# Kernel optimization log

Hardware: AMD Instinct MI355X
Metric: run time of the kernel (lower is better)

Reference implementation:

```python
import jax, jax.numpy as jnp
import numpy as np
import math

HIDDEN = 1024
ADAPTER = 256

def gelu_new(x):
    # BERT/GPT tanh-approx gelu, matches the torch code exactly
    return 0.5 * x * (1.0 + jnp.tanh(math.sqrt(2.0 / math.pi) * (x + 0.044715 * x ** 3)))

def setup_inputs() -> dict:
    key = jax.random.key(0)
    k1, k2, k3 = jax.random.split(key, 3)
    hidden_states = jax.random.normal(k1, (8, 4096, HIDDEN), dtype=jnp.float32)
    # LayerNorm params: weight=1, bias=0 per init_bert_weights
    ln_weight = jnp.ones((HIDDEN,), jnp.float32)
    ln_bias = jnp.zeros((HIDDEN,), jnp.float32)
    # Linear weights ~ N(0, 0.02), biases zero
    w_down = jax.random.normal(k2, (HIDDEN, ADAPTER), jnp.float32) * 0.02
    b_down = jnp.zeros((ADAPTER,), jnp.float32)
    w_up = jax.random.normal(k3, (ADAPTER, HIDDEN), jnp.float32) * 0.02
    b_up = jnp.zeros((HIDDEN,), jnp.float32)
    return {"hidden_states": hidden_states, "ln_weight": ln_weight, "ln_bias": ln_bias,
            "w_down": w_down, "b_down": b_down, "w_up": w_up, "b_up": b_up}

def layer_norm(x, weight, bias, eps=1e-5):
    mean = jnp.mean(x, axis=-1, keepdims=True)
    var = jnp.mean(jnp.square(x - mean), axis=-1, keepdims=True)
    return (x - mean) * jax.lax.rsqrt(var + eps) * weight + bias

def reference(hidden_states, ln_weight, ln_bias, w_down, b_down, w_up, b_up):
    h = layer_norm(hidden_states, ln_weight, ln_bias)           # [B,S,H]
    h = gelu_new(jnp.einsum('bsh,ha->bsa', h, w_down) + b_down)  # [B,S,A]
    h = jnp.einsum('bsa,ah->bsh', h, w_up) + b_up                # [B,S,H]
    return h + hidden_states
```

## Files before the change

kernel.cpp:

```cpp
#include <hip/hip_runtime.h>

#define HID 1024
#define ADP 256
#define MB  32

typedef short s16x8 __attribute__((ext_vector_type(8)));
typedef unsigned short u16x8 __attribute__((ext_vector_type(8)));
typedef float f32x4 __attribute__((ext_vector_type(4)));

__device__ __forceinline__ unsigned short f2bf(float f) {
    union { float f; unsigned int u; } v; v.f = f;
    unsigned int r = v.u + 0x7fffu + ((v.u >> 16) & 1u);
    return (unsigned short)(r >> 16);
}

__device__ __forceinline__ float bf2f(unsigned short u) {
    union { unsigned int u; float f; } v; v.u = ((unsigned int)u) << 16;
    return v.f;
}

__device__ __forceinline__ float gelu_new_f(float x) {
    float t = 0.7978845608028654f * x * (1.0f + 0.044715f * x * x);
    t = fminf(fmaxf(t, -15.f), 15.f);
    float e = __expf(-2.0f * t);
    float th = (1.0f - e) / (1.0f + e);
    return 0.5f * x * (1.0f + th);
}

__global__ void pack_b(const float* __restrict__ in, unsigned short* __restrict__ out,
                       const float* __restrict__ scale, int K, int N) {
    __shared__ unsigned short sh[32][72];
    int k0 = blockIdx.x * 32, n0 = blockIdx.y * 64;
    int t = threadIdx.x;
    int r = t >> 3, cg = t & 7;
    const float* src = in + (size_t)(k0 + r) * N + n0 + cg * 8;
    float sc = scale ? scale[k0 + r] : 1.0f;
    f32x4 v0 = *(const f32x4*)(src);
    f32x4 v1 = *(const f32x4*)(src + 4);
    #pragma unroll
    for (int e = 0; e < 4; ++e) {
        sh[r][cg * 8 + e]     = f2bf(sc * v0[e]);
        sh[r][cg * 8 + 4 + e] = f2bf(sc * v1[e]);
    }
    __syncthreads();
    int tile = t >> 6, l = t & 63, q = l >> 4, l15 = l & 15;
    u16x8 o;
    #pragma unroll
    for (int e = 0; e < 8; ++e)
        o[e] = sh[q * 8 + e][tile * 16 + l15];
    size_t tid_g = (size_t)(blockIdx.y * 4 + tile) * (K / 32) + blockIdx.x;
    *(u16x8*)(out + tid_g * 512 + (size_t)l * 8) = o;
}

__global__ void make_corr(const float* __restrict__ wd, const float* __restrict__ lnw,
                          const float* __restrict__ lnb, const float* __restrict__ bdn,
                          float* __restrict__ svec, float* __restrict__ tvec) {
    int w = threadIdx.x >> 6, lane = threadIdx.x & 63;
    int a = blockIdx.x * 4 + w;
    float sv = 0.f, tv = 0.f;
    #pragma unroll 4
    for (int i = 0; i < 16; ++i) {
        int h = lane + 64 * i;
        float wv_ = wd[(size_t)h * ADP + a];
        sv += bf2f(f2bf(lnw[h] * wv_));
        tv += lnb[h] * wv_;
    }
    #pragma unroll
    for (int s = 1; s < 64; s <<= 1) { sv += __shfl_xor(sv, s); tv += __shfl_xor(tv, s); }
    if (lane == 0) { svec[a] = sv; tvec[a] = bdn[a] + tv; }
}

__global__ __launch_bounds__(256, 4)
void adapter_fused(const float* __restrict__ x,
                   const float* __restrict__ bup,
                   const float* __restrict__ svec, const float* __restrict__ tvec,
                   const unsigned short* __restrict__ WdP,
                   const unsigned short* __restrict__ WuP,
                   float* __restrict__ out)
{
    __shared__ unsigned short a_h[MB][264];
    __shared__ float ep[4][16][68];
    __shared__ float stats[MB][2];
    __shared__ float sv_s[ADP], tv_s[ADP];

    const int tid  = threadIdx.x;
    const int wv   = tid >> 6;
    const int lane = tid & 63;
    const int q    = lane >> 4;
    const int l15  = lane & 15;
    const long row0 = (long)blockIdx.x * MB;

    sv_s[tid] = svec[tid];
    tv_s[tid] = tvec[tid];

    const int r   = tid >> 3;
    const int sub = tid & 7;

    f32x4 c1[2][4];
    #pragma unroll
    for (int a = 0; a < 2; ++a)
        #pragma unroll
        for (int b = 0; b < 4; ++b)
            c1[a][b] = (f32x4){0.f, 0.f, 0.f, 0.f};

    float sum1 = 0.f, sum2 = 0.f;

    f32x4 xv[8];
    {
        const f32x4* xr = (const f32x4*)(x + (row0 + r) * HID);
        #pragma unroll
        for (int i = 0; i < 8; ++i)
            xv[i] = __builtin_nontemporal_load(&xr[sub + 8 * i]);
    }

    for (int kc = 0; kc < 4; ++kc) {
        #pragma unroll
        for (int i = 0; i < 8; ++i) {
            int f4 = sub + 8 * i;
            f32x4 v = xv[i];
            sum1 += v[0] + v[1] + v[2] + v[3];
            sum2 += v[0] * v[0] + v[1] * v[1] + v[2] * v[2] + v[3] * v[3];
            ushort4 o;
            o.x = f2bf(v[0]); o.y = f2bf(v[1]); o.z = f2bf(v[2]); o.w = f2bf(v[3]);
            *(ushort4*)&a_h[r][f4 * 4] = o;
        }
        __syncthreads();
        if (kc < 3) {
            const f32x4* xr = (const f32x4*)(x + (row0 + r) * HID + (kc + 1) * 256);
            #pragma unroll
            for (int i = 0; i < 8; ++i)
                xv[i] = __builtin_nontemporal_load(&xr[sub + 8 * i]);
        }
        #pragma unroll
        for (int ks = 0; ks < 8; ++ks) {
            int kof = ks * 32 + q * 8;
            s16x8 af[2], bfr[4];
            af[0] = *(const s16x8*)&a_h[l15][kof];
            af[1] = *(const s16x8*)&a_h[16 + l15][kof];
            #pragma unroll
            for (int nt = 0; nt < 4; ++nt)
                bfr[nt] = *(const s16x8*)&WdP[(((size_t)(wv * 4 + nt) * 32) + kc * 8 + ks) * 512 + lane * 8];
            #pragma unroll
            for (int mt = 0; mt < 2; ++mt)
                #pragma unroll
                for (int nt = 0; nt < 4; ++nt)
                    c1[mt][nt] = __builtin_amdgcn_mfma_f32_16x16x32_bf16(af[mt], bfr[nt], c1[mt][nt], 0, 0, 0);
        }
        __syncthreads();
    }

    sum1 += __shfl_xor(sum1, 1); sum2 += __shfl_xor(sum2, 1);
    sum1 += __shfl_xor(sum1, 2); sum2 += __shfl_xor(sum2, 2);
    sum1 += __shfl_xor(sum1, 4); sum2 += __shfl_xor(sum2, 4);
    if (sub == 0) {
        float mean = sum1 * (1.f / HID);
        float var  = sum2 * (1.f / HID) - mean * mean;
        stats[r][0] = mean;
        stats[r][1] = rsqrtf(var + 1e-5f);
    }
    __syncthreads();

    #pragma unroll
    for (int mt = 0; mt < 2; ++mt)
        #pragma unroll
        for (int nt = 0; nt < 4; ++nt) {
            int a = wv * 64 + nt * 16 + l15;
            float sv = sv_s[a], tv = tv_s[a];
            #pragma unroll
            for (int rr = 0; rr < 4; ++rr) {
                int m = mt * 16 + q * 4 + rr;
                float mean = stats[m][0], rstd = stats[m][1];
                float c = rstd * (c1[mt][nt][rr] - mean * sv) + tv;
                a_h[m][a] = f2bf(gelu_new_f(c));
            }
        }
    __syncthreads();

    for (int ncc = 0; ncc < 4; ++ncc) {
        const int cb = wv * 256 + ncc * 64;
        f32x4 c2[2][4];
        #pragma unroll
        for (int a = 0; a < 2; ++a)
            #pragma unroll
            for (int b = 0; b < 4; ++b)
                c2[a][b] = (f32x4){0.f, 0.f, 0.f, 0.f};
        #pragma unroll
        for (int ks = 0; ks < 8; ++ks) {
            int kof = ks * 32 + q * 8;
            s16x8 af[2], bfr[4];
            af[0] = *(const s16x8*)&a_h[l15][kof];
            af[1] = *(const s16x8*)&a_h[16 + l15][kof];
            #pragma unroll
            for (int nt = 0; nt < 4; ++nt)
                bfr[nt] = *(const s16x8*)&WuP[(((size_t)(wv * 16 + ncc * 4 + nt) * 8) + ks) * 512 + lane * 8];
            #pragma unroll
            for (int mt = 0; mt < 2; ++mt)
                #pragma unroll
                for (int nt = 0; nt < 4; ++nt)
                    c2[mt][nt] = __builtin_amdgcn_mfma_f32_16x16x32_bf16(af[mt], bfr[nt], c2[mt][nt], 0, 0, 0);
        }
        #pragma unroll
        for (int mt = 0; mt < 2; ++mt) {
            #pragma unroll
            for (int nt = 0; nt < 4; ++nt)
                #pragma unroll
                for (int rr = 0; rr < 4; ++rr)
                    ep[wv][q * 4 + rr][nt * 16 + l15] = c2[mt][nt][rr];
            __builtin_amdgcn_s_waitcnt(0xc07f);
            int rr2 = lane >> 2, c4 = lane & 3;
            long gm = row0 + mt * 16 + rr2;
            const f32x4* xr = (const f32x4*)(x + gm * HID + cb);
            const f32x4* bu = (const f32x4*)(bup + cb);
            f32x4* orow     = (f32x4*)(out + gm * HID + cb);
            #pragma unroll
            for (int i = 0; i < 4; ++i) {
                int f4 = i * 4 + c4;
                f32x4 v  = *(const f32x4*)&ep[wv][rr2][f4 * 4];
                f32x4 rs = __builtin_nontemporal_load(&xr[f4]);
                f32x4 b4 = bu[f4];
                v += rs + b4;
                __builtin_nontemporal_store(v, &orow[f4]);
            }
            __builtin_amdgcn_s_waitcnt(0xc07f);
        }
    }
}

extern "C" void kernel_launch(void* const* d_in, const int* in_sizes, int n_in,
                              void* d_out, int out_size, void* d_ws, size_t ws_size,
                              hipStream_t stream) {
    const float* x   = (const float*)d_in[0];
    const float* lnw = (const float*)d_in[1];
    const float* lnb = (const float*)d_in[2];
    const float* wd  = (const float*)d_in[3];
    const float* bd  = (const float*)d_in[4];
    const float* wu  = (const float*)d_in[5];
    const float* bu  = (const float*)d_in[6];
    float* out = (float*)d_out;

    unsigned short* WdP = (unsigned short*)d_ws;
    unsigned short* WuP = WdP + (size_t)HID * ADP;
    float* svec = (float*)(WuP + (size_t)HID * ADP);
    float* tvec = svec + ADP;

    pack_b<<<dim3(HID / 32, ADP / 64), 256, 0, stream>>>(wd, WdP, lnw, HID, ADP);
    pack_b<<<dim3(ADP / 32, HID / 64), 256, 0, stream>>>(wu, WuP, nullptr, ADP, HID);
    make_corr<<<ADP / 4, 256, 0, stream>>>(wd, lnw, lnb, bd, svec, tvec);

    const int rows = in_sizes[0] / HID;
    adapter_fused<<<rows / MB, 256, 0, stream>>>(x, bu, svec, tvec, WdP, WuP, out);
}
```

Baseline: 338.9 us.

## Merge prep kernels and double fused-kernel block to 512 threads with direct epilogue

The three weight-preparation launches are merged into a single prep kernel, and the correction-vector pass now runs as one serial block. The fused adapter kernel moves from 256 to 512 threads per block, so each wave owns half as many output columns in both GEMMs and the per-wave accumulator registers shrink. The LDS staging epilogue is dropped in favour of scalar residual loads and stores straight from the MFMA layout. Input loads lose their nontemporal hint. The aim is more waves in flight and fewer launches, at the cost of narrower, less coalesced epilogue accesses and a slow serial correction block.

```diff
diff --git a/kernel.cpp b/kernel.cpp
--- a/kernel.cpp
+++ b/kernel.cpp
@@ -27,50 +27,52 @@
     return 0.5f * x * (1.0f + th);
 }
 
-__global__ void pack_b(const float* __restrict__ in, unsigned short* __restrict__ out,
-                       const float* __restrict__ scale, int K, int N) {
+__global__ __launch_bounds__(256)
+void prep(const float* __restrict__ wd, const float* __restrict__ wu,
+          const float* __restrict__ lnw, const float* __restrict__ lnb,
+          const float* __restrict__ bdn,
+          unsigned short* __restrict__ WdP, unsigned short* __restrict__ WuP,
+          float* __restrict__ svec, float* __restrict__ tvec)
+{
     __shared__ unsigned short sh[32][72];
-    int k0 = blockIdx.x * 32, n0 = blockIdx.y * 64;
-    int t = threadIdx.x;
-    int r = t >> 3, cg = t & 7;
-    const float* src = in + (size_t)(k0 + r) * N + n0 + cg * 8;
-    float sc = scale ? scale[k0 + r] : 1.0f;
-    f32x4 v0 = *(const f32x4*)(src);
-    f32x4 v1 = *(const f32x4*)(src + 4);
-    #pragma unroll
-    for (int e = 0; e < 4; ++e) {
-        sh[r][cg * 8 + e]     = f2bf(sc * v0[e]);
-        sh[r][cg * 8 + 4 + e] = f2bf(sc * v1[e]);
-    }
-    __syncthreads();
-    int tile = t >> 6, l = t & 63, q = l >> 4, l15 = l & 15;
-    u16x8 o;
-    #pragma unroll
-    for (int e = 0; e < 8; ++e)
-        o[e] = sh[q * 8 + e][tile * 16 + l15];
-    size_t tid_g = (size_t)(blockIdx.y * 4 + tile) * (K / 32) + blockIdx.x;
-    *(u16x8*)(out + tid_g * 512 + (size_t)l * 8) = o;
-}
-
-__global__ void make_corr(const float* __restrict__ wd, const float* __restrict__ lnw,
-                          const float* __restrict__ lnb, const float* __restrict__ bdn,
-                          float* __restrict__ svec, float* __restrict__ tvec) {
-    int w = threadIdx.x >> 6, lane = threadIdx.x & 63;
-    int a = blockIdx.x * 4 + w;
-    float sv = 0.f, tv = 0.f;
-    #pragma unroll 4
-    for (int i = 0; i < 16; ++i) {
-        int h = lane + 64 * i;
-        float wv_ = wd[(size_t)h * ADP + a];
-        sv += bf2f(f2bf(lnw[h] * wv_));
-        tv += lnb[h] * wv_;
-    }
-    #pragma unroll
-    for (int s = 1; s < 64; s <<= 1) { sv += __shfl_xor(sv, s); tv += __shfl_xor(tv, s); }
-    if (lane == 0) { svec[a] = sv; tvec[a] = bdn[a] + tv; }
-}
-
-__global__ __launch_bounds__(256, 4)
+    const int b = blockIdx.x, t = threadIdx.x;
+    if (b < 256) {
+        const float* in; unsigned short* outp; const float* scale; int K, N, kb, nb;
+        if (b < 128) { in = wd; outp = WdP; scale = lnw; K = HID; N = ADP; kb = b & 31; nb = b >> 5; }
+        else { int i = b - 128; in = wu; outp = WuP; scale = nullptr; K = ADP; N = HID; kb = i & 7; nb = i >> 3; }
+        const int k0 = kb * 32, n0 = nb * 64;
+        const int r = t >> 3, cg = t & 7;
+        const float* src = in + (size_t)(k0 + r) * N + n0 + cg * 8;
+        float sc = scale ? scale[k0 + r] : 1.0f;
+        f32x4 v0 = *(const f32x4*)(src);
+        f32x4 v1 = *(const f32x4*)(src + 4);
+        #pragma unroll
+        for (int e = 0; e < 4; ++e) {
+            sh[r][cg * 8 + e]     = f2bf(sc * v0[e]);
+            sh[r][cg * 8 + 4 + e] = f2bf(sc * v1[e]);
+        }
+        __syncthreads();
+        int tile = t >> 6, l = t & 63, q = l >> 4, l15 = l & 15;
+        u16x8 o;
+        #pragma unroll
+        for (int e = 0; e < 8; ++e)
+            o[e] = sh[q * 8 + e][tile * 16 + l15];
+        size_t tid_g = (size_t)(nb * 4 + tile) * (K / 32) + kb;
+        *(u16x8*)(outp + tid_g * 512 + (size_t)l * 8) = o;
+    } else {
+        float sv = 0.f, tv = 0.f;
+        #pragma unroll 8
+        for (int h = 0; h < HID; ++h) {
+            float w = wd[(size_t)h * ADP + t];
+            sv += bf2f(f2bf(lnw[h] * w));
+            tv += lnb[h] * w;
+        }
+        svec[t] = sv;
+        tvec[t] = bdn[t] + tv;
+    }
+}
+
+__global__ __launch_bounds__(512, 8)
 void adapter_fused(const float* __restrict__ x,
                    const float* __restrict__ bup,
                    const float* __restrict__ svec, const float* __restrict__ tvec,
@@ -79,7 +81,6 @@
                    float* __restrict__ out)
 {
     __shared__ unsigned short a_h[MB][264];
-    __shared__ float ep[4][16][68];
     __shared__ float stats[MB][2];
     __shared__ float sv_s[ADP], tv_s[ADP];
 
@@ -90,33 +91,32 @@
     const int l15  = lane & 15;
     const long row0 = (long)blockIdx.x * MB;
 
-    sv_s[tid] = svec[tid];
-    tv_s[tid] = tvec[tid];
-
-    const int r   = tid >> 3;
-    const int sub = tid & 7;
-
-    f32x4 c1[2][4];
+    if (tid < ADP) { sv_s[tid] = svec[tid]; tv_s[tid] = tvec[tid]; }
+
+    const int r   = tid >> 4;
+    const int sub = tid & 15;
+
+    f32x4 c1[2][2];
     #pragma unroll
     for (int a = 0; a < 2; ++a)
         #pragma unroll
-        for (int b = 0; b < 4; ++b)
-            c1[a][b] = (f32x4){0.f, 0.f, 0.f, 0.f};
+        for (int bb = 0; bb < 2; ++bb)
+            c1[a][bb] = (f32x4){0.f, 0.f, 0.f, 0.f};
 
     float sum1 = 0.f, sum2 = 0.f;
 
-    f32x4 xv[8];
+    f32x4 xv[4];
     {
         const f32x4* xr = (const f32x4*)(x + (row0 + r) * HID);
         #pragma unroll
-        for (int i = 0; i < 8; ++i)
-            xv[i] = __builtin_nontemporal_load(&xr[sub + 8 * i]);
+        for (int i = 0; i < 4; ++i)
+            xv[i] = xr[sub + 16 * i];
     }
 
     for (int kc = 0; kc < 4; ++kc) {
         #pragma unroll
-        for (int i = 0; i < 8; ++i) {
-            int f4 = sub + 8 * i;
+        for (int i = 0; i < 4; ++i) {
+            int f4 = sub + 16 * i;
             f32x4 v = xv[i];
             sum1 += v[0] + v[1] + v[2] + v[3];
             sum2 += v[0] * v[0] + v[1] * v[1] + v[2] * v[2] + v[3] * v[3];
@@ -128,22 +128,22 @@
         if (kc < 3) {
             const f32x4* xr = (const f32x4*)(x + (row0 + r) * HID + (kc + 1) * 256);
             #pragma unroll
-            for (int i = 0; i < 8; ++i)
-                xv[i] = __builtin_nontemporal_load(&xr[sub + 8 * i]);
+            for (int i = 0; i < 4; ++i)
+                xv[i] = xr[sub + 16 * i];
         }
         #pragma unroll
         for (int ks = 0; ks < 8; ++ks) {
             int kof = ks * 32 + q * 8;
-            s16x8 af[2], bfr[4];
+            s16x8 af[2], bfr[2];
             af[0] = *(const s16x8*)&a_h[l15][kof];
             af[1] = *(const s16x8*)&a_h[16 + l15][kof];
             #pragma unroll
-            for (int nt = 0; nt < 4; ++nt)
-                bfr[nt] = *(const s16x8*)&WdP[(((size_t)(wv * 4 + nt) * 32) + kc * 8 + ks) * 512 + lane * 8];
+            for (int nt = 0; nt < 2; ++nt)
+                bfr[nt] = *(const s16x8*)&WdP[(((size_t)(wv * 2 + nt) * 32) + kc * 8 + ks) * 512 + lane * 8];
             #pragma unroll
             for (int mt = 0; mt < 2; ++mt)
                 #pragma unroll
-                for (int nt = 0; nt < 4; ++nt)
+                for (int nt = 0; nt < 2; ++nt)
                     c1[mt][nt] = __builtin_amdgcn_mfma_f32_16x16x32_bf16(af[mt], bfr[nt], c1[mt][nt], 0, 0, 0);
         }
         __syncthreads();
@@ -152,6 +152,7 @@
     sum1 += __shfl_xor(sum1, 1); sum2 += __shfl_xor(sum2, 1);
     sum1 += __shfl_xor(sum1, 2); sum2 += __shfl_xor(sum2, 2);
     sum1 += __shfl_xor(sum1, 4); sum2 += __shfl_xor(sum2, 4);
+    sum1 += __shfl_xor(sum1, 8); sum2 += __shfl_xor(sum2, 8);
     if (sub == 0) {
         float mean = sum1 * (1.f / HID);
         float var  = sum2 * (1.f / HID) - mean * mean;
@@ -163,8 +164,8 @@
     #pragma unroll
     for (int mt = 0; mt < 2; ++mt)
         #pragma unroll
-        for (int nt = 0; nt < 4; ++nt) {
-            int a = wv * 64 + nt * 16 + l15;
+        for (int nt = 0; nt < 2; ++nt) {
+            int a = wv * 32 + nt * 16 + l15;
             float sv = sv_s[a], tv = tv_s[a];
             #pragma unroll
             for (int rr = 0; rr < 4; ++rr) {
@@ -176,14 +177,14 @@
         }
     __syncthreads();
 
-    for (int ncc = 0; ncc < 4; ++ncc) {
-        const int cb = wv * 256 + ncc * 64;
+    for (int ncc = 0; ncc < 2; ++ncc) {
+        const int cb = wv * 128 + ncc * 64;
         f32x4 c2[2][4];
         #pragma unroll
         for (int a = 0; a < 2; ++a)
             #pragma unroll
-            for (int b = 0; b < 4; ++b)
-                c2[a][b] = (f32x4){0.f, 0.f, 0.f, 0.f};
+            for (int bb = 0; bb < 4; ++bb)
+                c2[a][bb] = (f32x4){0.f, 0.f, 0.f, 0.f};
         #pragma unroll
         for (int ks = 0; ks < 8; ++ks) {
             int kof = ks * 32 + q * 8;
@@ -192,36 +193,28 @@
             af[1] = *(const s16x8*)&a_h[16 + l15][kof];
             #pragma unroll
             for (int nt = 0; nt < 4; ++nt)
-                bfr[nt] = *(const s16x8*)&WuP[(((size_t)(wv * 16 + ncc * 4 + nt) * 8) + ks) * 512 + lane * 8];
+                bfr[nt] = *(const s16x8*)&WuP[(((size_t)(wv * 8 + ncc * 4 + nt) * 8) + ks) * 512 + lane * 8];
             #pragma unroll
             for (int mt = 0; mt < 2; ++mt)
                 #pragma unroll
                 for (int nt = 0; nt < 4; ++nt)
                     c2[mt][nt] = __builtin_amdgcn_mfma_f32_16x16x32_bf16(af[mt], bfr[nt], c2[mt][nt], 0, 0, 0);
         }
+        float bu0[4];
+        #pragma unroll
+        for (int nt = 0; nt < 4; ++nt)
+            bu0[nt] = bup[cb + nt * 16 + l15];
         #pragma unroll
         for (int mt = 0; mt < 2; ++mt) {
+            size_t base = ((size_t)(row0 + mt * 16 + q * 4)) * HID + cb + l15;
             #pragma unroll
             for (int nt = 0; nt < 4; ++nt)
                 #pragma unroll
-                for (int rr = 0; rr < 4; ++rr)
-                    ep[wv][q * 4 + rr][nt * 16 + l15] = c2[mt][nt][rr];
-            __builtin_amdgcn_s_waitcnt(0xc07f);
-            int rr2 = lane >> 2, c4 = lane & 3;
-            long gm = row0 + mt * 16 + rr2;
-            const f32x4* xr = (const f32x4*)(x + gm * HID + cb);
-            const f32x4* bu = (const f32x4*)(bup + cb);
-            f32x4* orow     = (f32x4*)(out + gm * HID + cb);
-            #pragma unroll
-            for (int i = 0; i < 4; ++i) {
-                int f4 = i * 4 + c4;
-                f32x4 v  = *(const f32x4*)&ep[wv][rr2][f4 * 4];
-                f32x4 rs = __builtin_nontemporal_load(&xr[f4]);
-                f32x4 b4 = bu[f4];
-                v += rs + b4;
-                __builtin_nontemporal_store(v, &orow[f4]);
-            }
-            __builtin_amdgcn_s_waitcnt(0xc07f);
+                for (int rr = 0; rr < 4; ++rr) {
+                    size_t idx = base + (size_t)rr * HID + nt * 16;
+                    float v = c2[mt][nt][rr] + x[idx] + bu0[nt];
+                    __builtin_nontemporal_store(v, &out[idx]);
+                }
         }
     }
 }
@@ -243,10 +236,8 @@
     float* svec = (float*)(WuP + (size_t)HID * ADP);
     float* tvec = svec + ADP;
 
-    pack_b<<<dim3(HID / 32, ADP / 64), 256, 0, stream>>>(wd, WdP, lnw, HID, ADP);
-    pack_b<<<dim3(ADP / 32, HID / 64), 256, 0, stream>>>(wu, WuP, nullptr, ADP, HID);
-    make_corr<<<ADP / 4, 256, 0, stream>>>(wd, lnw, lnb, bd, svec, tvec);
+    prep<<<257, 256, 0, stream>>>(wd, wu, lnw, lnb, bd, WdP, WuP, svec, tvec);
 
     const int rows = in_sizes[0] / HID;
-    adapter_fused<<<rows / MB, 256, 0, stream>>>(x, bu, svec, tvec, WdP, WuP, out);
-}
+    adapter_fused<<<rows / MB, 512, 0, stream>>>(x, bu, svec, tvec, WdP, WuP, out);
+}
```

New measurement: 570.1 us. +68.2%, slower.
